# Performance work log

Measured on AMD Instinct MI355X. Metric: run time of the kernel, lower is better.

The kernel has to match this reference:

```python
import jax, jax.numpy as jnp
import numpy as np

B, S, H, R = 2, 4096, 2048, 2048
NB, CW = 16, 4
BW = R // NB


def _block_diag_linear(x, w, b):
    # x: [B,S,R]; w: [NB,BW,BW]; b: [NB,BW]
    xb = x.reshape(x.shape[0], x.shape[1], NB, BW)
    out = jnp.einsum('bsni,nij->bsnj', xb, w) + b
    return out.reshape(x.shape)


def _causal_conv1d(x, conv_w, conv_b):
    # depthwise causal temporal conv: out[t] = sum_i w[i]*x[t-CW+1+i] + b
    xp = jnp.pad(x, ((0, 0), (CW - 1, 0), (0, 0)))
    out = conv_b
    for i in range(CW):
        out = out + conv_w[i] * xp[:, i:i + x.shape[1], :]
    return out


def _rg_lru_scan(x, x_gate_pre, a_gate_pre, a_param):
    gate_x = jax.nn.sigmoid(x_gate_pre)
    gate_a = jax.nn.sigmoid(a_gate_pre)
    log_a = -8.0 * gate_a * jax.nn.softplus(a_param)  # [B,S,R]
    a = jnp.exp(log_a)
    multiplier = jnp.sqrt(-jnp.expm1(2.0 * log_a))  # sqrt(1 - a^2)
    norm_x = x * gate_x * multiplier
    # h_t = a_t * h_{t-1} + norm_x_t via parallel associative scan over time
    def combine(c1, c2):
        a1, b1 = c1
        a2, b2 = c2
        return a1 * a2, a2 * b1 + b2
    _, h = jax.lax.associative_scan(combine, (a, norm_x), axis=1)
    return h


def setup_inputs() -> dict:
    key = jax.random.key(0)
    ks = jax.random.split(key, 9)
    x = jax.random.normal(ks[0], (B, S, H), dtype=jnp.float32)
    W_xy = jax.random.normal(ks[1], (2 * R, H), dtype=jnp.float32) / np.sqrt(H)
    ig_w = jax.random.normal(ks[2], (NB, BW, BW), dtype=jnp.float32) / np.sqrt(BW)
    ig_b = jnp.zeros((NB, BW), dtype=jnp.float32)
    ag_w = jax.random.normal(ks[3], (NB, BW, BW), dtype=jnp.float32) / np.sqrt(BW)
    ag_b = jnp.zeros((NB, BW), dtype=jnp.float32)
    # forget_init: a = a_real in [0.9, 0.999]; a_param = softplus^{-1}(-log(a_real))
    unif = jax.random.uniform(ks[4], (R,), dtype=jnp.float32)
    a_real = 0.5 * jnp.log(unif * (0.999 ** 2 - 0.9 ** 2) + 0.9 ** 2 + 1e-8)
    a_param = jnp.log(jnp.expm1(-a_real))
    conv_w = jax.random.normal(ks[5], (CW, R), dtype=jnp.float32) / np.sqrt(CW * R)
    conv_b = jnp.zeros((R,), dtype=jnp.float32)
    # resid_proj is zero-init in the module; use small random so output is non-trivial
    W_resid = 0.02 * jax.random.normal(ks[6], (H, R), dtype=jnp.float32)
    return {"x": x, "W_xy": W_xy, "ig_w": ig_w, "ig_b": ig_b,
            "ag_w": ag_w, "ag_b": ag_b, "a_param": a_param,
            "conv_w": conv_w, "conv_b": conv_b, "W_resid": W_resid}


def reference(x, W_xy, ig_w, ig_b, ag_w, ag_b, a_param, conv_w, conv_b, W_resid):
    xy = jnp.einsum('bsh,rh->bsr', x, W_xy)  # [B,S,2R]
    xr, y = jnp.split(xy, 2, axis=-1)
    xc = _causal_conv1d(xr, conv_w, conv_b)
    x_gate_pre = _block_diag_linear(xc, ig_w, ig_b)
    a_gate_pre = _block_diag_linear(xc, ag_w, ag_b)
    h = _rg_lru_scan(xc, x_gate_pre, a_gate_pre, a_param)
    out = jnp.einsum('bsr,hr->bsh', jax.nn.gelu(y, approximate=False) * h, W_resid)
    return out
```

## Files before the change

kernel.cpp:

```cpp
#include <hip/hip_runtime.h>
#include <hip/hip_bf16.h>

typedef __hip_bfloat16 bf16;
typedef __attribute__((ext_vector_type(8))) short s16x8;
typedef __attribute__((ext_vector_type(4))) float f32x4;

#define B_ 2
#define S_ 4096
#define H_ 2048
#define R_ 2048
#define M_ 8192
#define NB_ 16
#define BW_ 128
#define CHUNK 64
#define NCH 64

__device__ __forceinline__ short f2b_s(float f) {
    return (short)__builtin_bit_cast(unsigned short, __float2bfloat16(f));
}
__device__ __forceinline__ float b2f_s(short s) {
    unsigned int u = ((unsigned int)(unsigned short)s) << 16;
    return __builtin_bit_cast(float, u);
}
__device__ __forceinline__ float sigm_fast(float x) { return 1.f / (1.f + __expf(-x)); }

__device__ __forceinline__ void async_g2l(const void* g, void* l) {
    __builtin_amdgcn_global_load_lds((const __attribute__((address_space(1))) void*)g,
                                     (__attribute__((address_space(3))) void*)l, 16, 0, 0);
}

__global__ __launch_bounds__(256) void cast_all(const float* __restrict__ x,
                                                const float* __restrict__ wxy,
                                                const float* __restrict__ wres,
                                                bf16* __restrict__ xbf,
                                                bf16* __restrict__ wxyb,
                                                bf16* __restrict__ wresb) {
    int idx = blockIdx.x * 256 + threadIdx.x;
    const float* in; bf16* out; int off;
    if (idx < 2097152)      { in = x;    out = xbf;   off = idx; }
    else if (idx < 3145728) { in = wxy;  out = wxyb;  off = idx - 2097152; }
    else                    { in = wres; out = wresb; off = idx - 3145728; }
    size_t i8 = (size_t)off * 8;
    float4 v0 = *(const float4*)(in + i8);
    float4 v1 = *(const float4*)(in + i8 + 4);
    s16x8 o;
    o[0] = f2b_s(v0.x); o[1] = f2b_s(v0.y); o[2] = f2b_s(v0.z); o[3] = f2b_s(v0.w);
    o[4] = f2b_s(v1.x); o[5] = f2b_s(v1.y); o[6] = f2b_s(v1.z); o[7] = f2b_s(v1.w);
    *(s16x8*)(out + i8) = o;
}

__global__ __launch_bounds__(256) void wcast_T(const float* __restrict__ igw,
                                               const float* __restrict__ agw,
                                               bf16* __restrict__ wT) {
    __shared__ float tile[128 * 129];
    int blk = blockIdx.x;
    int p = blk >> 4, n = blk & 15;
    const float* w = (p ? agw : igw) + (size_t)n * 16384;
    int tid = threadIdx.x;
#pragma unroll
    for (int it = 0; it < 64; ++it) {
        int u = it * 256 + tid;
        tile[(u >> 7) * 129 + (u & 127)] = w[u];
    }
    __syncthreads();
    bf16* o = wT + (size_t)blk * 16384;
#pragma unroll
    for (int it = 0; it < 64; ++it) {
        int u = it * 256 + tid;
        o[u] = __float2bfloat16(tile[(u & 127) * 129 + (u >> 7)]);
    }
}

__global__ __launch_bounds__(256) void sp8_kernel(const float* __restrict__ apar,
                                                  float* __restrict__ sp8) {
    int r = blockIdx.x * 256 + threadIdx.x;
    float ap = apar[r];
    sp8[r] = 8.f * (ap > 20.f ? ap : log1pf(expf(ap)));
}

__device__ __forceinline__ void store_c(float* p, float v) { *p = v; }
__device__ __forceinline__ void store_c(bf16* p, float v) { *p = __float2bfloat16(v); }

template <typename OutT>
__global__ __launch_bounds__(512, 2) void gemm256(const bf16* __restrict__ A,
                                                  const bf16* __restrict__ Bm,
                                                  OutT* __restrict__ C,
                                                  int K, int lda, int ldb, int ldc) {
    extern __shared__ __align__(16) char lds[];
    const int tid = threadIdx.x;
    const int lane = tid & 63, wave = tid >> 6;
    const int wm = wave >> 2, wn = wave & 3;
    const int fm = lane & 15, q = lane >> 4;
    const int mBase = blockIdx.y * 256, nBase = blockIdx.x * 256;
    const int NT = K >> 6;

    auto stage_unit = [&](int k) {
        if (k >= 4 * NT) return;
        const int tt = k >> 2, hh = k & 3;
        const bf16* src = (hh & 1) ? Bm : A;
        const int ld = (hh & 1) ? ldb : lda;
        const int rowBase = (hh & 1) ? nBase : mBase;
        char* dst = lds + ((tt & 1) << 16) + (hh << 14);
        const int kcol = tt * 64 + (hh >> 1) * 32;
#pragma unroll
        for (int rnd = 0; rnd < 2; ++rnd) {
            int off = rnd * 8192 + tid * 16;
            int r = off >> 6;
            int g = ((off >> 4) & 3) ^ ((r >> 1) & 3);
            async_g2l(src + (size_t)(rowBase + r) * ld + kcol + g * 8, dst + off);
        }
    };

    f32x4 acc[8][4];
#pragma unroll
    for (int i = 0; i < 8; ++i)
#pragma unroll
        for (int j = 0; j < 4; ++j) acc[i][j] = (f32x4){0.f, 0.f, 0.f, 0.f};

#pragma unroll
    for (int k = 0; k < 6; ++k) stage_unit(k);
    asm volatile("s_waitcnt vmcnt(8)" ::: "memory");
    __builtin_amdgcn_s_barrier();
    __builtin_amdgcn_sched_barrier(0);

    for (int T = 0; T < NT; ++T) {
        const int buf = T & 1;
        const char* base = lds + (buf << 16);
        s16x8 bfr[4];
#pragma unroll
        for (int p = 0; p < 4; ++p) {
            const int ks = p >> 1, sub = p & 1;
            if (sub == 0) {
#pragma unroll
                for (int j = 0; j < 4; ++j) {
                    int row = wn * 64 + j * 16 + fm;
                    bfr[j] = *(const s16x8*)(base + 16384 + (ks << 15) + row * 64 +
                                             ((q ^ ((row >> 1) & 3)) << 4));
                }
            }
            s16x8 af[4];
#pragma unroll
            for (int i2 = 0; i2 < 4; ++i2) {
                int row = wm * 128 + (sub * 4 + i2) * 16 + fm;
                af[i2] = *(const s16x8*)(base + (ks << 15) + row * 64 +
                                         ((q ^ ((row >> 1) & 3)) << 4));
            }
            stage_unit(4 * T + 6 + p);
            __builtin_amdgcn_s_barrier();
            asm volatile("s_waitcnt lgkmcnt(0)" ::: "memory");
            __builtin_amdgcn_sched_barrier(0);
            __builtin_amdgcn_s_setprio(1);
#pragma unroll
            for (int i2 = 0; i2 < 4; ++i2)
#pragma unroll
                for (int j = 0; j < 4; ++j)
                    acc[sub * 4 + i2][j] = __builtin_amdgcn_mfma_f32_16x16x32_bf16(
                        af[i2], bfr[j], acc[sub * 4 + i2][j], 0, 0, 0);
            __builtin_amdgcn_s_setprio(0);
            if (p == 1) {
                if (T < NT - 1) asm volatile("s_waitcnt vmcnt(8)" ::: "memory");
                else            asm volatile("s_waitcnt vmcnt(0)" ::: "memory");
            } else if (p == 3) {
                if (T < NT - 2)       asm volatile("s_waitcnt vmcnt(8)" ::: "memory");
                else if (T == NT - 2) asm volatile("s_waitcnt vmcnt(4)" ::: "memory");
            }
            __builtin_amdgcn_s_barrier();
            __builtin_amdgcn_sched_barrier(0);
        }
    }

#pragma unroll
    for (int i = 0; i < 8; ++i) {
        int rowg = mBase + wm * 128 + i * 16 + q * 4;
#pragma unroll
        for (int j = 0; j < 4; ++j) {
            int colg = nBase + wn * 64 + j * 16 + fm;
#pragma unroll
            for (int rr = 0; rr < 4; ++rr)
                store_c(C + (size_t)(rowg + rr) * ldc + colg, acc[i][j][rr]);
        }
    }
}

__global__ __launch_bounds__(256) void gate_kernel(const bf16* __restrict__ xy,
                                                   const float* __restrict__ cw,
                                                   const float* __restrict__ cb,
                                                   const bf16* __restrict__ wT,
                                                   const float* __restrict__ igb,
                                                   const float* __restrict__ agb,
                                                   const float* __restrict__ sp8,
                                                   bf16* __restrict__ la_out,
                                                   bf16* __restrict__ nx_out,
                                                   float* __restrict__ Ach,
                                                   float* __restrict__ Hla) {
    __shared__ __align__(16) short As[64 * 128];
    __shared__ __align__(16) char  Wmem[128 * 256];
    short* Xs   = (short*)Wmem;
    short* Ws   = (short*)Wmem;
    float* a_sh = (float*)Wmem;
    const int n = blockIdx.x;
    const int mBase = blockIdx.y * 64;
    const int tid = threadIdx.x;
    const int lane = tid & 63, wave = tid >> 6;
    const int fm = lane & 15, q = lane >> 4;
    const int t0 = mBase & (S_ - 1);

#pragma unroll
    for (int it = 0; it < 5; ++it) {
        int u = it * 256 + tid;
        if (u < 67 * 16) {
            int rr = u >> 4, gg = u & 15;
            s16x8 v = (s16x8){0, 0, 0, 0, 0, 0, 0, 0};
            if (t0 != 0 || rr >= 3) {
                int m = mBase + rr - 3;
                v = *(const s16x8*)(xy + (size_t)m * 4096 + n * BW_ + gg * 8);
            }
            *(s16x8*)((char*)Xs + u * 16) = v;
        }
    }
    __syncthreads();

    {
        int col = tid & 127, rh = tid >> 7;
        int rbase = n * BW_ + col;
        float w0c = cw[rbase], w1c = cw[R_ + rbase], w2c = cw[2 * R_ + rbase],
              w3c = cw[3 * R_ + rbase];
        float bc = cb[rbase];
        int r0 = rh * 32;
        float xm3 = b2f_s(Xs[(r0 + 0) * 128 + col]);
        float xm2 = b2f_s(Xs[(r0 + 1) * 128 + col]);
        float xm1 = b2f_s(Xs[(r0 + 2) * 128 + col]);
#pragma unroll
        for (int rw = 0; rw < 32; ++rw) {
            int row = r0 + rw;
            float x0 = b2f_s(Xs[(row + 3) * 128 + col]);
            float v = bc + w0c * xm3 + w1c * xm2 + w2c * xm1 + w3c * x0;
            xm3 = xm2; xm2 = xm1; xm1 = x0;
            *(short*)((char*)As + row * 256 + ((((col >> 3)) ^ (row & 15)) << 4) +
                      (col & 7) * 2) = f2b_s(v);
        }
    }
    __syncthreads();

    const bf16* w0 = wT + (size_t)n * 16384;
#pragma unroll
    for (int it = 0; it < 8; ++it) {
        int off = it * 4096 + tid * 16;
        int j = off >> 8;
        int g = ((off & 255) >> 4) ^ (j & 15);
        async_g2l(w0 + j * 128 + g * 8, (char*)Ws + off);
    }
    __syncthreads();

    f32x4 accI[8], accA[8];
#pragma unroll
    for (int jj = 0; jj < 8; ++jj) {
        accI[jj] = (f32x4){0.f, 0.f, 0.f, 0.f};
        accA[jj] = (f32x4){0.f, 0.f, 0.f, 0.f};
    }

    const int row = wave * 16 + fm;
#pragma unroll
    for (int s = 0; s < 4; ++s) {
        s16x8 af = *(const s16x8*)((char*)As + row * 256 + ((((s << 2) + q) ^ (row & 15)) << 4));
#pragma unroll
        for (int jj = 0; jj < 8; ++jj) {
            int wrow = jj * 16 + fm;
            s16x8 bw = *(const s16x8*)((char*)Ws + wrow * 256 + ((((s << 2) + q) ^ (wrow & 15)) << 4));
            accI[jj] = __builtin_amdgcn_mfma_f32_16x16x32_bf16(af, bw, accI[jj], 0, 0, 0);
        }
    }
    __syncthreads();
    const bf16* w1 = wT + (size_t)(NB_ + n) * 16384;
#pragma unroll
    for (int it = 0; it < 8; ++it) {
        int off = it * 4096 + tid * 16;
        int j = off >> 8;
        int g = ((off & 255) >> 4) ^ (j & 15);
        async_g2l(w1 + j * 128 + g * 8, (char*)Ws + off);
    }
    __syncthreads();
#pragma unroll
    for (int s = 0; s < 4; ++s) {
        s16x8 af = *(const s16x8*)((char*)As + row * 256 + ((((s << 2) + q) ^ (row & 15)) << 4));
#pragma unroll
        for (int jj = 0; jj < 8; ++jj) {
            int wrow = jj * 16 + fm;
            s16x8 bw = *(const s16x8*)((char*)Ws + wrow * 256 + ((((s << 2) + q) ^ (wrow & 15)) << 4));
            accA[jj] = __builtin_amdgcn_mfma_f32_16x16x32_bf16(af, bw, accA[jj], 0, 0, 0);
        }
    }
    __syncthreads();

#pragma unroll
    for (int jj = 0; jj < 8; ++jj) {
        int col = jj * 16 + fm;
        int r = n * BW_ + col;
        float bi = igb[r], ba = agb[r];
        float s8 = sp8[r];
#pragma unroll
        for (int rr = 0; rr < 4; ++rr) {
            int rowl = wave * 16 + q * 4 + rr;
            short* slot = (short*)((char*)As + rowl * 256 +
                          ((((col >> 3)) ^ (rowl & 15)) << 4) + (col & 7) * 2);
            float xcv = b2f_s(*slot);
            float xg = accI[jj][rr] + bi;
            float ag = accA[jj][rr] + ba;
            float la = -s8 * sigm_fast(ag);
            float av = __expf(la);
            float t2 = 2.f * la;
            float nem = (t2 > -0.125f)
                ? -t2 * (1.f + t2 * (0.5f + t2 * (0.16666667f + t2 * 0.04166667f)))
                : 1.f - av * av;
            float nxv = xcv * sigm_fast(xg) * sqrtf(nem);
            short nxs = f2b_s(nxv);
            size_t o = (size_t)(mBase + rowl) * R_ + r;
            la_out[o] = __float2bfloat16(la);
            nx_out[o] = __builtin_bit_cast(bf16, (unsigned short)nxs);
            a_sh[rowl * 128 + col] = av;
            *slot = nxs;
        }
    }
    __syncthreads();

    if (tid < 128) {
        int col = tid;
        float h = 0.f, cum = 1.f;
#pragma unroll 4
        for (int t = 0; t < CHUNK; ++t) {
            float a = a_sh[t * 128 + col];
            float nxv = b2f_s(*(const short*)((char*)As + t * 256 +
                              ((((col >> 3)) ^ (t & 15)) << 4) + (col & 7) * 2));
            h = fmaf(a, h, nxv);
            cum *= a;
        }
        int b = mBase >> 12, c = (mBase & (S_ - 1)) >> 6;
        int so = ((b * NCH + c) << 11) + n * BW_ + col;
        Ach[so] = cum;
        Hla[so] = h;
    }
}

__global__ __launch_bounds__(256) void scan_carry(const float* __restrict__ Ach,
                                                  const float* __restrict__ Hla,
                                                  float* __restrict__ carry) {
    int idx = blockIdx.x * 256 + threadIdx.x;
    int r = idx & (R_ - 1), b = idx >> 11;
    float cy = 0.f;
    for (int c = 0; c < NCH; ++c) {
        int o = (b * NCH + c) * R_ + r;
        carry[o] = cy;
        cy = fmaf(Ach[o], cy, Hla[o]);
    }
}

__global__ __launch_bounds__(256) void scan_passB(const bf16* __restrict__ la_buf,
                                                  const bf16* __restrict__ nx_buf,
                                                  const float* __restrict__ carry,
                                                  const bf16* __restrict__ xy,
                                                  bf16* __restrict__ g_out) {
    int bid = blockIdx.x;
    int rt = bid & 7, c = (bid >> 3) & 63, b = bid >> 9;
    int r = rt * 256 + threadIdx.x;
    int m0 = b * S_ + c * CHUNK;
    size_t base = (size_t)m0 * R_ + r;
    const bf16* yp = xy + (size_t)m0 * 4096 + 2048 + r;
    int so = (b * NCH + c) * R_ + r;
    float h = carry[so];
    for (int t = 0; t < CHUNK; ++t) {
        size_t o = base + (size_t)t * R_;
        float a = __expf(__bfloat162float(la_buf[o]));
        float nx = __bfloat162float(nx_buf[o]);
        h = fmaf(a, h, nx);
        float y = __bfloat162float(yp[(size_t)t * 4096]);
        float g = 0.5f * y * (1.f + erff(y * 0.70710678f));
        g_out[o] = __float2bfloat16(g * h);
    }
}

extern "C" void kernel_launch(void* const* d_in, const int* in_sizes, int n_in,
                              void* d_out, int out_size, void* d_ws, size_t ws_size,
                              hipStream_t stream) {
    const float* x    = (const float*)d_in[0];
    const float* Wxy  = (const float*)d_in[1];
    const float* igw  = (const float*)d_in[2];
    const float* igb  = (const float*)d_in[3];
    const float* agw  = (const float*)d_in[4];
    const float* agb  = (const float*)d_in[5];
    const float* apar = (const float*)d_in[6];
    const float* cw   = (const float*)d_in[7];
    const float* cb   = (const float*)d_in[8];
    const float* Wres = (const float*)d_in[9];
    float* out = (float*)d_out;

    char* ws = (char*)d_ws;
    const size_t MiB = (size_t)1 << 20;
    bf16*  xbf   = (bf16*)(ws);
    bf16*  la    = (bf16*)(ws);
    bf16*  wxyb  = (bf16*)(ws + 32 * MiB);
    bf16*  wT    = (bf16*)(ws + 32 * MiB);
    float* sp8   = (float*)(ws + 33 * MiB + 65536);
    bf16*  xy    = (bf16*)(ws + 48 * MiB);
    bf16*  wresb = (bf16*)(ws + 112 * MiB);
    bf16*  g     = (bf16*)(ws + 120 * MiB);
    bf16*  nx    = (bf16*)(ws + 152 * MiB);
    float* Ach   = (float*)(ws + 184 * MiB);
    float* Hla   = (float*)(ws + 185 * MiB);
    float* cyb   = (float*)(ws + 186 * MiB);

    cast_all<<<14336, 256, 0, stream>>>(x, Wxy, Wres, xbf, wxyb, wresb);

    gemm256<bf16><<<dim3(16, 32), 512, 131072, stream>>>(xbf, wxyb, xy, 2048, 2048, 2048, 4096);

    wcast_T<<<32, 256, 0, stream>>>(igw, agw, wT);
    sp8_kernel<<<8, 256, 0, stream>>>(apar, sp8);

    gate_kernel<<<dim3(NB_, 128), 256, 0, stream>>>(xy, cw, cb, wT, igb, agb, sp8,
                                                    la, nx, Ach, Hla);

    scan_carry<<<16, 256, 0, stream>>>(Ach, Hla, cyb);
    scan_passB<<<1024, 256, 0, stream>>>(la, nx, cyb, xy, g);

    gemm256<float><<<dim3(8, 32), 512, 131072, stream>>>(g, wresb, out, 2048, 2048, 2048, 2048);
}
```

Baseline: 471.9 us.

## Double-buffer LDS fragment reads in GEMM to overlap with MFMA

Restructures the GEMM main loop so each phase issues LDS reads for the next sub-tile's A/B fragments into a second register set before running the MFMAs on the current fragments. The next K-tile's first fragments are prefetched at the end of the iteration. vmcnt waits are tightened from 8 to 4 outstanding loads to match the new staging order. The aim is to hide LDS latency behind matrix ops. The cost is more registers (doubled fragments), and the waits and barriers are delicate, with some risk to correctness.

```diff
diff --git a/kernel.cpp b/kernel.cpp
--- a/kernel.cpp
+++ b/kernel.cpp
@@ -111,6 +111,23 @@
         }
     };
 
+    auto rdA = [&](const char* base, int ks, int sub, s16x8* dst) {
+#pragma unroll
+        for (int i2 = 0; i2 < 4; ++i2) {
+            int row = wm * 128 + (sub * 4 + i2) * 16 + fm;
+            dst[i2] = *(const s16x8*)(base + (ks << 15) + row * 64 +
+                                      ((q ^ ((row >> 1) & 3)) << 4));
+        }
+    };
+    auto rdB = [&](const char* base, int ks, s16x8* dst) {
+#pragma unroll
+        for (int j = 0; j < 4; ++j) {
+            int row = wn * 64 + j * 16 + fm;
+            dst[j] = *(const s16x8*)(base + 16384 + (ks << 15) + row * 64 +
+                                     ((q ^ ((row >> 1) & 3)) << 4));
+        }
+    };
+
     f32x4 acc[8][4];
 #pragma unroll
     for (int i = 0; i < 8; ++i)
@@ -119,54 +136,87 @@
 
 #pragma unroll
     for (int k = 0; k < 6; ++k) stage_unit(k);
-    asm volatile("s_waitcnt vmcnt(8)" ::: "memory");
+    asm volatile("s_waitcnt vmcnt(4)" ::: "memory");
     __builtin_amdgcn_s_barrier();
     __builtin_amdgcn_sched_barrier(0);
 
+    s16x8 afC[4], afN[4], bfC[4], bfN[4];
+    rdA(lds, 0, 0, afC);
+    rdB(lds, 0, bfC);
+
     for (int T = 0; T < NT; ++T) {
-        const int buf = T & 1;
-        const char* base = lds + (buf << 16);
-        s16x8 bfr[4];
-#pragma unroll
-        for (int p = 0; p < 4; ++p) {
-            const int ks = p >> 1, sub = p & 1;
-            if (sub == 0) {
-#pragma unroll
-                for (int j = 0; j < 4; ++j) {
-                    int row = wn * 64 + j * 16 + fm;
-                    bfr[j] = *(const s16x8*)(base + 16384 + (ks << 15) + row * 64 +
-                                             ((q ^ ((row >> 1) & 3)) << 4));
-                }
-            }
-            s16x8 af[4];
-#pragma unroll
-            for (int i2 = 0; i2 < 4; ++i2) {
-                int row = wm * 128 + (sub * 4 + i2) * 16 + fm;
-                af[i2] = *(const s16x8*)(base + (ks << 15) + row * 64 +
-                                         ((q ^ ((row >> 1) & 3)) << 4));
-            }
-            stage_unit(4 * T + 6 + p);
-            __builtin_amdgcn_s_barrier();
-            asm volatile("s_waitcnt lgkmcnt(0)" ::: "memory");
-            __builtin_amdgcn_sched_barrier(0);
-            __builtin_amdgcn_s_setprio(1);
-#pragma unroll
-            for (int i2 = 0; i2 < 4; ++i2)
-#pragma unroll
-                for (int j = 0; j < 4; ++j)
-                    acc[sub * 4 + i2][j] = __builtin_amdgcn_mfma_f32_16x16x32_bf16(
-                        af[i2], bfr[j], acc[sub * 4 + i2][j], 0, 0, 0);
-            __builtin_amdgcn_s_setprio(0);
-            if (p == 1) {
-                if (T < NT - 1) asm volatile("s_waitcnt vmcnt(8)" ::: "memory");
-                else            asm volatile("s_waitcnt vmcnt(0)" ::: "memory");
-            } else if (p == 3) {
-                if (T < NT - 2)       asm volatile("s_waitcnt vmcnt(8)" ::: "memory");
-                else if (T == NT - 2) asm volatile("s_waitcnt vmcnt(4)" ::: "memory");
-            }
-            __builtin_amdgcn_s_barrier();
-            __builtin_amdgcn_sched_barrier(0);
-        }
+        const char* base  = lds + ((T & 1) << 16);
+        const char* baseN = lds + (((T + 1) & 1) << 16);
+
+        stage_unit(4 * T + 6);
+        __builtin_amdgcn_s_barrier();
+        asm volatile("s_waitcnt lgkmcnt(0)" ::: "memory");
+        __builtin_amdgcn_sched_barrier(0);
+        rdA(base, 0, 1, afN);
+        __builtin_amdgcn_s_setprio(1);
+#pragma unroll
+        for (int i2 = 0; i2 < 4; ++i2)
+#pragma unroll
+            for (int j = 0; j < 4; ++j)
+                acc[i2][j] = __builtin_amdgcn_mfma_f32_16x16x32_bf16(
+                    afC[i2], bfC[j], acc[i2][j], 0, 0, 0);
+        __builtin_amdgcn_s_setprio(0);
+        __builtin_amdgcn_s_barrier();
+        __builtin_amdgcn_sched_barrier(0x7);
+
+        stage_unit(4 * T + 7);
+        __builtin_amdgcn_s_barrier();
+        asm volatile("s_waitcnt lgkmcnt(0)" ::: "memory");
+        __builtin_amdgcn_sched_barrier(0);
+        rdA(base, 1, 0, afC);
+        rdB(base, 1, bfN);
+        __builtin_amdgcn_s_setprio(1);
+#pragma unroll
+        for (int i2 = 0; i2 < 4; ++i2)
+#pragma unroll
+            for (int j = 0; j < 4; ++j)
+                acc[4 + i2][j] = __builtin_amdgcn_mfma_f32_16x16x32_bf16(
+                    afN[i2], bfC[j], acc[4 + i2][j], 0, 0, 0);
+        __builtin_amdgcn_s_setprio(0);
+        if (T < NT - 1) asm volatile("s_waitcnt vmcnt(4)" ::: "memory");
+        else            asm volatile("s_waitcnt vmcnt(0)" ::: "memory");
+        __builtin_amdgcn_s_barrier();
+        __builtin_amdgcn_sched_barrier(0x7);
+
+        stage_unit(4 * T + 8);
+        __builtin_amdgcn_s_barrier();
+        asm volatile("s_waitcnt lgkmcnt(0)" ::: "memory");
+        __builtin_amdgcn_sched_barrier(0);
+        rdA(base, 1, 1, afN);
+        __builtin_amdgcn_s_setprio(1);
+#pragma unroll
+        for (int i2 = 0; i2 < 4; ++i2)
+#pragma unroll
+            for (int j = 0; j < 4; ++j)
+                acc[i2][j] = __builtin_amdgcn_mfma_f32_16x16x32_bf16(
+                    afC[i2], bfN[j], acc[i2][j], 0, 0, 0);
+        __builtin_amdgcn_s_setprio(0);
+        __builtin_amdgcn_s_barrier();
+        __builtin_amdgcn_sched_barrier(0x7);
+
+        stage_unit(4 * T + 9);
+        __builtin_amdgcn_s_barrier();
+        asm volatile("s_waitcnt lgkmcnt(0)" ::: "memory");
+        __builtin_amdgcn_sched_barrier(0);
+        rdA(baseN, 0, 0, afC);
+        rdB(baseN, 0, bfC);
+        __builtin_amdgcn_s_setprio(1);
+#pragma unroll
+        for (int i2 = 0; i2 < 4; ++i2)
+#pragma unroll
+            for (int j = 0; j < 4; ++j)
+                acc[4 + i2][j] = __builtin_amdgcn_mfma_f32_16x16x32_bf16(
+                    afN[i2], bfN[j], acc[4 + i2][j], 0, 0, 0);
+        __builtin_amdgcn_s_setprio(0);
+        if (T < NT - 2) asm volatile("s_waitcnt vmcnt(4)" ::: "memory");
+        else            asm volatile("s_waitcnt vmcnt(0)" ::: "memory");
+        __builtin_amdgcn_s_barrier();
+        __builtin_amdgcn_sched_barrier(0x7);
     }
 
 #pragma unroll
```

New measurement: 462.2 us. -2.1%, faster.
